# Performance work log

Measured on AMD Instinct MI355X. Metric: run time of the kernel, lower is better.

The kernel has to match this reference:

```python
import jax, jax.numpy as jnp
import numpy as np

H = 16
MAX_SEQ_LEN = 2048
B = 1
S = 2048


def setup_inputs() -> dict:
    key = jax.random.key(0)
    k1, k2, k3 = jax.random.split(key, 3)
    # int8-valued attention scores (stored as int32; values centered in [-64, 63])
    x_q = jax.random.randint(k1, (B, H, S, S), 0, 127, dtype=jnp.int32) - 64
    # per-(head, row) dequant scale for the scores
    scale_x = 0.005 + 0.015 * jax.random.uniform(k2, (H, MAX_SEQ_LEN), dtype=jnp.float32)
    # per-(head, row) requant scale for the softmax output (probs in [0,1], so ~1/127)
    scale_out = 0.004 + 0.006 * jax.random.uniform(k3, (H, MAX_SEQ_LEN), dtype=jnp.float32)
    return {"x_q": x_q, "scale_x": scale_x, "scale_out": scale_out}


def reference(x_q, scale_x, scale_out):
    seq_len = x_q.shape[-1]
    sx = scale_x[:, :seq_len]   # [H, S] per-row dequant scale
    so = scale_out[:, :seq_len]  # [H, S] per-row requant scale
    # dequantize: x[b,h,i,j] = x_q[b,h,i,j] * sx[h,i]
    x = x_q.astype(jnp.float32) * sx[None, :, :, None]
    # causal (tril) mask over the last dim
    mask = jnp.tril(jnp.ones((seq_len, seq_len), dtype=bool))  # [S, S]
    logits = jnp.where(mask[None, None, :, :], x, -jnp.inf)
    p = jax.nn.softmax(logits, axis=-1)
    # symmetric int8 requantization with per-(head, row) scale
    out_q = jnp.clip(jnp.round(p / so[None, :, :, None]), -128, 127).astype(jnp.int8)
    return (out_q, so)
```

## Files before the change

kernel.cpp:

```cpp
#include <hip/hip_runtime.h>
#include <math.h>

constexpr int S = 2048;
constexpr int HS = 16 * S;
constexpr long long OUTQ_ELEMS = (long long)HS * S;

typedef int   vint4   __attribute__((ext_vector_type(4)));
typedef float vfloat4 __attribute__((ext_vector_type(4)));

__global__ __launch_bounds__(256) void softmax_quant_row_kernel(
    const int*   __restrict__ x_q,
    const float* __restrict__ scale_x,
    const float* __restrict__ scale_out,
    float*       __restrict__ out_q,
    float*       __restrict__ so_out)
{
    const int row = blockIdx.x;
    const int i   = row & (S - 1);
    const int tid = threadIdx.x;

    const float sx = scale_x[row];
    const float so = scale_out[row];

    const int*  rowp = x_q   + (size_t)row * S;
    float*      outp = out_q + (size_t)row * S;

    const int j0 = tid * 4;
    const int j1 = j0 + (S / 2);

    vint4 q0 = (vint4)(0);
    vint4 q1 = (vint4)(0);
    if (j0 <= i) q0 = __builtin_nontemporal_load(
                        reinterpret_cast<const vint4*>(rowp + j0));
    if (j1 <= i) q1 = __builtin_nontemporal_load(
                        reinterpret_cast<const vint4*>(rowp + j1));

    const float c = sx * 1.4426950408889634f;

    float e[8];
    e[0] = (j0 + 0 <= i) ? __builtin_amdgcn_exp2f((float)q0.x * c) : 0.0f;
    e[1] = (j0 + 1 <= i) ? __builtin_amdgcn_exp2f((float)q0.y * c) : 0.0f;
    e[2] = (j0 + 2 <= i) ? __builtin_amdgcn_exp2f((float)q0.z * c) : 0.0f;
    e[3] = (j0 + 3 <= i) ? __builtin_amdgcn_exp2f((float)q0.w * c) : 0.0f;
    e[4] = (j1 + 0 <= i) ? __builtin_amdgcn_exp2f((float)q1.x * c) : 0.0f;
    e[5] = (j1 + 1 <= i) ? __builtin_amdgcn_exp2f((float)q1.y * c) : 0.0f;
    e[6] = (j1 + 2 <= i) ? __builtin_amdgcn_exp2f((float)q1.z * c) : 0.0f;
    e[7] = (j1 + 3 <= i) ? __builtin_amdgcn_exp2f((float)q1.w * c) : 0.0f;
    float s = ((e[0] + e[1]) + (e[2] + e[3])) + ((e[4] + e[5]) + (e[6] + e[7]));

    #pragma unroll
    for (int off = 32; off > 0; off >>= 1)
        s += __shfl_xor(s, off, 64);

    __shared__ float redsum[4];
    const int wave = tid >> 6;
    if ((tid & 63) == 0) redsum[wave] = s;
    __syncthreads();
    s = (redsum[0] + redsum[1]) + (redsum[2] + redsum[3]);

    const float scale = 1.0f / (s * so);

    vfloat4 o0, o1;
    o0.x = fminf(fmaxf(rintf(e[0] * scale), -128.0f), 127.0f);
    o0.y = fminf(fmaxf(rintf(e[1] * scale), -128.0f), 127.0f);
    o0.z = fminf(fmaxf(rintf(e[2] * scale), -128.0f), 127.0f);
    o0.w = fminf(fmaxf(rintf(e[3] * scale), -128.0f), 127.0f);
    o1.x = fminf(fmaxf(rintf(e[4] * scale), -128.0f), 127.0f);
    o1.y = fminf(fmaxf(rintf(e[5] * scale), -128.0f), 127.0f);
    o1.z = fminf(fmaxf(rintf(e[6] * scale), -128.0f), 127.0f);
    o1.w = fminf(fmaxf(rintf(e[7] * scale), -128.0f), 127.0f);

    __builtin_nontemporal_store(o0, reinterpret_cast<vfloat4*>(outp + j0));
    __builtin_nontemporal_store(o1, reinterpret_cast<vfloat4*>(outp + j1));

    if (tid == 0) so_out[row] = so;
}

extern "C" void kernel_launch(void* const* d_in, const int* in_sizes, int n_in,
                              void* d_out, int out_size, void* d_ws, size_t ws_size,
                              hipStream_t stream) {
    const int*   x_q       = (const int*)d_in[0];
    const float* scale_x   = (const float*)d_in[1];
    const float* scale_out = (const float*)d_in[2];

    float* out    = (float*)d_out;
    float* so_out = out + OUTQ_ELEMS;

    dim3 grid(HS);
    dim3 block(256);
    softmax_quant_row_kernel<<<grid, block, 0, stream>>>(
        x_q, scale_x, scale_out, out, so_out);
}
```

Before: 70.23 us.

## Map one softmax row per wavefront to drop block-level reduction and barrier

```diff
diff --git a/kernel.cpp b/kernel.cpp
--- a/kernel.cpp
+++ b/kernel.cpp
@@ -8,72 +8,73 @@
 typedef int   vint4   __attribute__((ext_vector_type(4)));
 typedef float vfloat4 __attribute__((ext_vector_type(4)));
 
-__global__ __launch_bounds__(256) void softmax_quant_row_kernel(
+__global__ __launch_bounds__(256) void softmax_quant_wave_kernel(
     const int*   __restrict__ x_q,
     const float* __restrict__ scale_x,
     const float* __restrict__ scale_out,
     float*       __restrict__ out_q,
     float*       __restrict__ so_out)
 {
-    const int row = blockIdx.x;
-    const int i   = row & (S - 1);
-    const int tid = threadIdx.x;
+    const int tid  = threadIdx.x;
+    const int lane = tid & 63;
+    const int wave = tid >> 6;
+    const int row  = blockIdx.x * 4 + wave;
+    const int i    = row & (S - 1);
 
     const float sx = scale_x[row];
     const float so = scale_out[row];
+    const float c  = sx * 1.4426950408889634f;
 
     const int*  rowp = x_q   + (size_t)row * S;
     float*      outp = out_q + (size_t)row * S;
 
-    const int j0 = tid * 4;
-    const int j1 = j0 + (S / 2);
+    float e[8][4];
+    float s = 0.0f;
 
-    vint4 q0 = (vint4)(0);
-    vint4 q1 = (vint4)(0);
-    if (j0 <= i) q0 = __builtin_nontemporal_load(
+    #pragma unroll
+    for (int ch = 0; ch < 8; ++ch) {
+        const int jb = ch * 256;
+        const int j0 = jb + lane * 4;
+        if (jb + 255 <= i) {
+            vint4 q = __builtin_nontemporal_load(
                         reinterpret_cast<const vint4*>(rowp + j0));
-    if (j1 <= i) q1 = __builtin_nontemporal_load(
-                        reinterpret_cast<const vint4*>(rowp + j1));
-
-    const float c = sx * 1.4426950408889634f;
-
-    float e[8];
-    e[0] = (j0 + 0 <= i) ? __builtin_amdgcn_exp2f((float)q0.x * c) : 0.0f;
-    e[1] = (j0 + 1 <= i) ? __builtin_amdgcn_exp2f((float)q0.y * c) : 0.0f;
-    e[2] = (j0 + 2 <= i) ? __builtin_amdgcn_exp2f((float)q0.z * c) : 0.0f;
-    e[3] = (j0 + 3 <= i) ? __builtin_amdgcn_exp2f((float)q0.w * c) : 0.0f;
-    e[4] = (j1 + 0 <= i) ? __builtin_amdgcn_exp2f((float)q1.x * c) : 0.0f;
-    e[5] = (j1 + 1 <= i) ? __builtin_amdgcn_exp2f((float)q1.y * c) : 0.0f;
-    e[6] = (j1 + 2 <= i) ? __builtin_amdgcn_exp2f((float)q1.z * c) : 0.0f;
-    e[7] = (j1 + 3 <= i) ? __builtin_amdgcn_exp2f((float)q1.w * c) : 0.0f;
-    float s = ((e[0] + e[1]) + (e[2] + e[3])) + ((e[4] + e[5]) + (e[6] + e[7]));
+            e[ch][0] = __builtin_amdgcn_exp2f((float)q.x * c);
+            e[ch][1] = __builtin_amdgcn_exp2f((float)q.y * c);
+            e[ch][2] = __builtin_amdgcn_exp2f((float)q.z * c);
+            e[ch][3] = __builtin_amdgcn_exp2f((float)q.w * c);
+            s += (e[ch][0] + e[ch][1]) + (e[ch][2] + e[ch][3]);
+        } else if (jb <= i) {
+            vint4 q = (vint4)(0);
+            if (j0 <= i) q = __builtin_nontemporal_load(
+                               reinterpret_cast<const vint4*>(rowp + j0));
+            e[ch][0] = (j0 + 0 <= i) ? __builtin_amdgcn_exp2f((float)q.x * c) : 0.0f;
+            e[ch][1] = (j0 + 1 <= i) ? __builtin_amdgcn_exp2f((float)q.y * c) : 0.0f;
+            e[ch][2] = (j0 + 2 <= i) ? __builtin_amdgcn_exp2f((float)q.z * c) : 0.0f;
+            e[ch][3] = (j0 + 3 <= i) ? __builtin_amdgcn_exp2f((float)q.w * c) : 0.0f;
+            s += (e[ch][0] + e[ch][1]) + (e[ch][2] + e[ch][3]);
+        } else {
+            e[ch][0] = 0.0f; e[ch][1] = 0.0f; e[ch][2] = 0.0f; e[ch][3] = 0.0f;
+        }
+    }
 
     #pragma unroll
     for (int off = 32; off > 0; off >>= 1)
         s += __shfl_xor(s, off, 64);
 
-    __shared__ float redsum[4];
-    const int wave = tid >> 6;
-    if ((tid & 63) == 0) redsum[wave] = s;
-    __syncthreads();
-    s = (redsum[0] + redsum[1]) + (redsum[2] + redsum[3]);
-
     const float scale = 1.0f / (s * so);
 
-    vfloat4 o0, o1;
-    o0.x = fminf(fmaxf(rintf(e[0] * scale), -128.0f), 127.0f);
-    o0.y = fminf(fmaxf(rintf(e[1] * scale), -128.0f), 127.0f);
-    o0.z = fminf(fmaxf(rintf(e[2] * scale), -128.0f), 127.0f);
-    o0.w = fminf(fmaxf(rintf(e[3] * scale), -128.0f), 127.0f);
-    o1.x = fminf(fmaxf(rintf(e[4] * scale), -128.0f), 127.0f);
-    o1.y = fminf(fmaxf(rintf(e[5] * scale), -128.0f), 127.0f);
-    o1.z = fminf(fmaxf(rintf(e[6] * scale), -128.0f), 127.0f);
-    o1.w = fminf(fmaxf(rintf(e[7] * scale), -128.0f), 127.0f);
+    #pragma unroll
+    for (int ch = 0; ch < 8; ++ch) {
+        const int j0 = ch * 256 + lane * 4;
+        vfloat4 o;
+        o.x = fminf(rintf(e[ch][0] * scale), 127.0f);
+        o.y = fminf(rintf(e[ch][1] * scale), 127.0f);
+        o.z = fminf(rintf(e[ch][2] * scale), 127.0f);
+        o.w = fminf(rintf(e[ch][3] * scale), 127.0f);
+        __builtin_nontemporal_store(o, reinterpret_cast<vfloat4*>(outp + j0));
+    }
 
-    __builtin_nontemporal_store(o0, reinterpret_cast<vfloat4*>(outp + j0));
-    __builtin_nontemporal_store(o1, reinterpret_cast<vfloat4*>(outp + j1));
-
-    if (tid == 0) so_out[row] = so;
+    if (lane == 0) so_out[row] = so;
 }
 
 extern "C" void kernel_launch(void* const* d_in, const int* in_sizes, int n_in,
@@ -86,8 +87,8 @@
     float* out    = (float*)d_out;
     float* so_out = out + OUTQ_ELEMS;
 
-    dim3 grid(HS);
+    dim3 grid(HS / 4);
     dim3 block(256);
-    softmax_quant_row_kernel<<<grid, block, 0, stream>>>(
+    softmax_quant_wave_kernel<<<grid, block, 0, stream>>>(
         x_q, scale_x, scale_out, out, so_out);
 }
```

Result: slower. 76.96 us (+9.6%).
